# Optimization experiments

Hardware: AMD Instinct MI355X
Metric: run time of the kernel (lower is better)

The kernel has to match this reference:

```python
import jax, jax.numpy as jnp
import numpy as np

N = 50000          # nodes
E = 800000         # edges (avg in-degree 16)
IN_FEATS = 256
H = 4              # num_heads
D = 32             # out_feats per head
NEG_SLOPE = 0.2


def setup_inputs() -> dict:
    key = jax.random.key(0)
    k1, k2, k3, k4, k5, k6 = jax.random.split(key, 6)
    feat = jax.random.normal(k1, (N, IN_FEATS), dtype=jnp.float32)
    src = jax.random.randint(k2, (E,), 0, N, dtype=jnp.int32)
    dst = jax.random.randint(k3, (E,), 0, N, dtype=jnp.int32)
    # parameters (xavier-ish scale)
    W = jax.random.normal(k4, (IN_FEATS, H * D), dtype=jnp.float32) * (2.0 / (IN_FEATS + H * D)) ** 0.5
    attn_l = jax.random.normal(k5, (H, D), dtype=jnp.float32) * 0.1
    attn_r = jax.random.normal(k6, (H, D), dtype=jnp.float32) * 0.1
    bias = jnp.zeros((H * D,), dtype=jnp.float32)
    return {"feat": feat, "src": src, "dst": dst, "W": W,
            "attn_l": attn_l, "attn_r": attn_r, "bias": bias}


def reference(feat, src, dst, W, attn_l, attn_r, bias):
    # dense projection: [N, H, D]
    ft = (feat @ W).reshape(N, H, D)
    # per-node attention logits: [N, H]
    el = jnp.einsum('nhd,hd->nh', ft, attn_l)
    er = jnp.einsum('nhd,hd->nh', ft, attn_r)
    # SDDMM u_add_v + leaky relu: per-edge scores [E, H]
    e = jax.nn.leaky_relu(el[src] + er[dst], negative_slope=NEG_SLOPE)
    # edge softmax over incoming edges of each dst node (segment softmax)
    m = jax.ops.segment_max(e, dst, num_segments=N)          # [N, H], -inf for empty
    e_exp = jnp.exp(e - m[dst])                               # [E, H]
    s = jax.ops.segment_sum(e_exp, dst, num_segments=N)       # [N, H]
    a = e_exp / s[dst]                                        # [E, H]
    # SpMM u_mul_e: weighted aggregation to dst nodes
    rst = jax.ops.segment_sum(ft[src] * a[:, :, None], dst, num_segments=N)  # [N, H, D]
    rst = rst + bias.reshape(1, H, D)
    return rst
```

## Files before the change

### kernel.cpp

```cpp
#include <hip/hip_runtime.h>
#include <hip/hip_bf16.h>
#include <math.h>

#define N_NODES 50000
#define N_EDGES 800000
#define IN_F 256
#define HD 128
#define NHEAD 4
#define NB_SCAN 196

typedef __attribute__((ext_vector_type(8))) short bf16x8;
typedef __attribute__((ext_vector_type(4))) float f32x4;

__device__ __forceinline__ float lrelu(float x){ return x > 0.f ? x : 0.2f * x; }

__device__ __forceinline__ unsigned short f32_to_bf16_rn(float x){
    union { float f; unsigned int u; } v; v.f = x;
    unsigned int r = v.u + 0x7FFFu + ((v.u >> 16) & 1u);
    return (unsigned short)(r >> 16);
}
__device__ __forceinline__ float bf16_to_f32(unsigned short h){
    union { unsigned int u; float f; } v; v.u = ((unsigned int)h) << 16;
    return v.f;
}
__device__ __forceinline__ float bflo(unsigned int u){
    union { unsigned int x; float f; } v; v.x = u << 16; return v.f;
}
__device__ __forceinline__ float bfhi(unsigned int u){
    union { unsigned int x; float f; } v; v.x = u & 0xFFFF0000u; return v.f;
}

__global__ void zero_ints(int* __restrict__ p, int n){
    int i = blockIdx.x * blockDim.x + threadIdx.x;
    if (i < n) p[i] = 0;
}

__global__ __launch_bounds__(256) void wsplit_kernel(const float* __restrict__ W,
                                                     unsigned short* __restrict__ Wt_hi,
                                                     unsigned short* __restrict__ Wt_lo){
    int gid = blockIdx.x * 256 + threadIdx.x;
    int n = gid >> 8;
    int k = gid & 255;
    float x = W[(size_t)k * HD + n];
    unsigned short h = f32_to_bf16_rn(x);
    float r = x - bf16_to_f32(h);
    unsigned short l = f32_to_bf16_rn(r);
    Wt_hi[gid] = h;
    Wt_lo[gid] = l;
}

__global__ __launch_bounds__(256) void gemm_kernel(const float* __restrict__ feat,
                                                   const unsigned short* __restrict__ Wt_hi,
                                                   const unsigned short* __restrict__ Wt_lo,
                                                   const float* __restrict__ attn_l,
                                                   const float* __restrict__ attn_r,
                                                   unsigned short* __restrict__ ftb,
                                                   float* __restrict__ el,
                                                   float* __restrict__ er){
    __shared__ unsigned short Ah[128][72];
    __shared__ unsigned short Al[128][72];
    __shared__ unsigned short Bh[128][72];
    __shared__ unsigned short Bl[128][72];

    const int tid  = threadIdx.x;
    const int lane = tid & 63;
    const int wave = tid >> 6;
    const int wrow = wave * 32;
    const int lrow = lane & 15;
    const int lkh  = (lane >> 4) * 8;
    const int row0 = blockIdx.x * 128;

    f32x4 acc[2][8];
#pragma unroll
    for (int i = 0; i < 2; i++)
#pragma unroll
        for (int j = 0; j < 8; j++) acc[i][j] = (f32x4){0.f, 0.f, 0.f, 0.f};

    const int srow = tid >> 1;
    const int skh  = (tid & 1) * 32;

    for (int kc = 0; kc < 4; ++kc){
        const int k0 = kc * 64;
        {
            int gr = row0 + srow;
            const float* fp = feat + (size_t)gr * IN_F + k0 + skh;
            unsigned short* ah = &Ah[srow][skh];
            unsigned short* al = &Al[srow][skh];
#pragma unroll
            for (int u = 0; u < 8; ++u){
                float4 v = make_float4(0.f,0.f,0.f,0.f);
                if (gr < N_NODES) v = *(const float4*)(fp + 4 * u);
                ushort4 h, l;
                h.x = f32_to_bf16_rn(v.x); l.x = f32_to_bf16_rn(v.x - bf16_to_f32(h.x));
                h.y = f32_to_bf16_rn(v.y); l.y = f32_to_bf16_rn(v.y - bf16_to_f32(h.y));
                h.z = f32_to_bf16_rn(v.z); l.z = f32_to_bf16_rn(v.z - bf16_to_f32(h.z));
                h.w = f32_to_bf16_rn(v.w); l.w = f32_to_bf16_rn(v.w - bf16_to_f32(h.w));
                *(ushort4*)(ah + 4 * u) = h;
                *(ushort4*)(al + 4 * u) = l;
            }
        }
        {
            const unsigned short* bh = Wt_hi + srow * 256 + k0 + skh;
            const unsigned short* bl = Wt_lo + srow * 256 + k0 + skh;
#pragma unroll
            for (int u = 0; u < 4; ++u){
                *(uint4*)(&Bh[srow][skh + 8 * u]) = *(const uint4*)(bh + 8 * u);
                *(uint4*)(&Bl[srow][skh + 8 * u]) = *(const uint4*)(bl + 8 * u);
            }
        }
        __syncthreads();
#pragma unroll
        for (int kk = 0; kk < 2; ++kk){
            const int kb = kk * 32 + lkh;
            bf16x8 ah0 = *(const bf16x8*)(&Ah[wrow + lrow][kb]);
            bf16x8 ah1 = *(const bf16x8*)(&Ah[wrow + 16 + lrow][kb]);
            bf16x8 al0 = *(const bf16x8*)(&Al[wrow + lrow][kb]);
            bf16x8 al1 = *(const bf16x8*)(&Al[wrow + 16 + lrow][kb]);
#pragma unroll
            for (int nf = 0; nf < 8; ++nf){
                bf16x8 bh = *(const bf16x8*)(&Bh[nf * 16 + lrow][kb]);
                bf16x8 bl = *(const bf16x8*)(&Bl[nf * 16 + lrow][kb]);
                acc[0][nf] = __builtin_amdgcn_mfma_f32_16x16x32_bf16(ah0, bh, acc[0][nf], 0, 0, 0);
                acc[1][nf] = __builtin_amdgcn_mfma_f32_16x16x32_bf16(ah1, bh, acc[1][nf], 0, 0, 0);
                acc[0][nf] = __builtin_amdgcn_mfma_f32_16x16x32_bf16(ah0, bl, acc[0][nf], 0, 0, 0);
                acc[1][nf] = __builtin_amdgcn_mfma_f32_16x16x32_bf16(ah1, bl, acc[1][nf], 0, 0, 0);
                acc[0][nf] = __builtin_amdgcn_mfma_f32_16x16x32_bf16(al0, bh, acc[0][nf], 0, 0, 0);
                acc[1][nf] = __builtin_amdgcn_mfma_f32_16x16x32_bf16(al1, bh, acc[1][nf], 0, 0, 0);
            }
        }
        __syncthreads();
    }
    float alv[8], arv[8];
#pragma unroll
    for (int nf = 0; nf < 8; ++nf){
        alv[nf] = attn_l[lrow + nf * 16];
        arv[nf] = attn_r[lrow + nf * 16];
    }
#pragma unroll
    for (int mf = 0; mf < 2; ++mf){
#pragma unroll
        for (int r = 0; r < 4; ++r){
            int gr = row0 + wrow + mf * 16 + (lane >> 4) * 4 + r;
            if (gr < N_NODES){
                unsigned short* op = ftb + (size_t)gr * HD + lrow;
#pragma unroll
                for (int nf = 0; nf < 8; ++nf) op[nf * 16] = f32_to_bf16_rn(acc[mf][nf][r]);
            }
            float pl0 = acc[mf][0][r] * alv[0] + acc[mf][1][r] * alv[1];
            float pl1 = acc[mf][2][r] * alv[2] + acc[mf][3][r] * alv[3];
            float pl2 = acc[mf][4][r] * alv[4] + acc[mf][5][r] * alv[5];
            float pl3 = acc[mf][6][r] * alv[6] + acc[mf][7][r] * alv[7];
            float pr0 = acc[mf][0][r] * arv[0] + acc[mf][1][r] * arv[1];
            float pr1 = acc[mf][2][r] * arv[2] + acc[mf][3][r] * arv[3];
            float pr2 = acc[mf][4][r] * arv[4] + acc[mf][5][r] * arv[5];
            float pr3 = acc[mf][6][r] * arv[6] + acc[mf][7][r] * arv[7];
#pragma unroll
            for (int m = 1; m <= 8; m <<= 1){
                pl0 += __shfl_xor(pl0, m, 64); pl1 += __shfl_xor(pl1, m, 64);
                pl2 += __shfl_xor(pl2, m, 64); pl3 += __shfl_xor(pl3, m, 64);
                pr0 += __shfl_xor(pr0, m, 64); pr1 += __shfl_xor(pr1, m, 64);
                pr2 += __shfl_xor(pr2, m, 64); pr3 += __shfl_xor(pr3, m, 64);
            }
            if ((lane & 15) == 0 && gr < N_NODES){
                *(float4*)(el + (size_t)gr * NHEAD) = make_float4(pl0, pl1, pl2, pl3);
                *(float4*)(er + (size_t)gr * NHEAD) = make_float4(pr0, pr1, pr2, pr3);
            }
        }
    }
}

__global__ void degree_kernel(const int* __restrict__ dst, int* __restrict__ deg){
    int e = blockIdx.x * blockDim.x + threadIdx.x;
    if (e < N_EDGES) atomicAdd(&deg[dst[e]], 1);
}

__global__ __launch_bounds__(256) void scan_part(const int* __restrict__ deg,
                                                 int* __restrict__ row_off,
                                                 int* __restrict__ blk_sums){
    __shared__ int lds[256];
    int tid = threadIdx.x;
    int i = blockIdx.x * 256 + tid;
    int v = (i < N_NODES) ? deg[i] : 0;
    int x = v;
    lds[tid] = x;
    __syncthreads();
    for (int off = 1; off < 256; off <<= 1){
        int t = (tid >= off) ? lds[tid - off] : 0;
        __syncthreads();
        x += t;
        lds[tid] = x;
        __syncthreads();
    }
    if (i < N_NODES) row_off[i] = x - v;
    if (tid == 255) blk_sums[blockIdx.x] = x;
}

__global__ __launch_bounds__(256) void scan_mid(int* __restrict__ blk_sums,
                                                int* __restrict__ blk_off){
    __shared__ int lds[256];
    int tid = threadIdx.x;
    int v = (tid < NB_SCAN) ? blk_sums[tid] : 0;
    int x = v;
    lds[tid] = x;
    __syncthreads();
    for (int off = 1; off < 256; off <<= 1){
        int t = (tid >= off) ? lds[tid - off] : 0;
        __syncthreads();
        x += t;
        lds[tid] = x;
        __syncthreads();
    }
    blk_off[tid] = x - v;
}

__global__ __launch_bounds__(256) void scan_add(int* __restrict__ row_off,
                                                const int* __restrict__ blk_off){
    int i = blockIdx.x * 256 + threadIdx.x;
    if (i < N_NODES) row_off[i] += blk_off[blockIdx.x];
    if (blockIdx.x == 0 && threadIdx.x == 0) row_off[N_NODES] = N_EDGES;
}

__global__ void scatter_kernel(const int* __restrict__ src, const int* __restrict__ dst,
                               const float* __restrict__ el, const float* __restrict__ er,
                               const int* __restrict__ row_off, int* __restrict__ cursor,
                               int* __restrict__ csr_src, float* __restrict__ w_srt){
    int e = blockIdx.x * blockDim.x + threadIdx.x;
    if (e >= N_EDGES) return;
    int d = dst[e], s = src[e];
    int pos = row_off[d] + atomicAdd(&cursor[d], 1);
    csr_src[pos] = s;
    float4 elv = *(const float4*)(el + (size_t)s * NHEAD);
    float4 erv = *(const float4*)(er + (size_t)d * NHEAD);
    float4 w;
    w.x = __expf(lrelu(elv.x + erv.x));
    w.y = __expf(lrelu(elv.y + erv.y));
    w.z = __expf(lrelu(elv.z + erv.z));
    w.w = __expf(lrelu(elv.w + erv.w));
    *(float4*)(w_srt + (size_t)pos * NHEAD) = w;
}

__global__ __launch_bounds__(256) void aggregate_kernel(const unsigned short* __restrict__ ftb,
                                                        const int* __restrict__ csr_src,
                                                        const float* __restrict__ w_srt,
                                                        const int* __restrict__ row_off,
                                                        const float* __restrict__ bias,
                                                        float* __restrict__ out){
    int n    = blockIdx.x * 4 + (threadIdx.x >> 6);
    int lane = threadIdx.x & 63;
    int h    = lane >> 4;
    int beg  = row_off[n], end = row_off[n + 1];

    float a0 = 0.f, a1 = 0.f, ws = 0.f;
    int i = beg;
    for (; i + 4 <= end; i += 4){
        int s0 = csr_src[i + 0], s1 = csr_src[i + 1], s2 = csr_src[i + 2], s3 = csr_src[i + 3];
        float w0 = w_srt[(size_t)(i + 0) * NHEAD + h];
        float w1 = w_srt[(size_t)(i + 1) * NHEAD + h];
        float w2 = w_srt[(size_t)(i + 2) * NHEAD + h];
        float w3 = w_srt[(size_t)(i + 3) * NHEAD + h];
        unsigned int f0 = *(const unsigned int*)(ftb + (size_t)s0 * HD + 2 * lane);
        unsigned int f1 = *(const unsigned int*)(ftb + (size_t)s1 * HD + 2 * lane);
        unsigned int f2 = *(const unsigned int*)(ftb + (size_t)s2 * HD + 2 * lane);
        unsigned int f3 = *(const unsigned int*)(ftb + (size_t)s3 * HD + 2 * lane);
        a0 += w0 * bflo(f0) + w1 * bflo(f1) + w2 * bflo(f2) + w3 * bflo(f3);
        a1 += w0 * bfhi(f0) + w1 * bfhi(f1) + w2 * bfhi(f2) + w3 * bfhi(f3);
        ws += (w0 + w1) + (w2 + w3);
    }
    for (; i < end; ++i){
        int s = csr_src[i];
        float w = w_srt[(size_t)i * NHEAD + h];
        unsigned int f = *(const unsigned int*)(ftb + (size_t)s * HD + 2 * lane);
        a0 += w * bflo(f);
        a1 += w * bfhi(f);
        ws += w;
    }
    float inv = (end > beg) ? 1.f / ws : 0.f;
    float2 o;
    o.x = a0 * inv + bias[2 * lane + 0];
    o.y = a1 * inv + bias[2 * lane + 1];
    *(float2*)(out + (size_t)n * HD + 2 * lane) = o;
}

extern "C" void kernel_launch(void* const* d_in, const int* in_sizes, int n_in,
                              void* d_out, int out_size, void* d_ws, size_t ws_size,
                              hipStream_t stream){
    const float* feat   = (const float*)d_in[0];
    const int*   src    = (const int*)  d_in[1];
    const int*   dst    = (const int*)  d_in[2];
    const float* W      = (const float*)d_in[3];
    const float* attn_l = (const float*)d_in[4];
    const float* attn_r = (const float*)d_in[5];
    const float* bias   = (const float*)d_in[6];
    float* out = (float*)d_out;
    char*  ws  = (char*)d_ws;

    unsigned short* ftb = (unsigned short*)(ws + 0);
    float* el      = (float*)(ws + 12800000);
    float* er      = (float*)(ws + 13600000);
    int*   deg     = (int*)  (ws + 14400000);
    int*   cursor  = (int*)  (ws + 14600000);
    int*   row_off = (int*)  (ws + 14800000);
    int*   csr_src = (int*)  (ws + 15000064);
    float* w_srt   = (float*)(ws + 18200064);

    unsigned short* Wt_hi = (unsigned short*)csr_src;
    unsigned short* Wt_lo = Wt_hi + 32768;
    int* blk_sums = (int*)w_srt;
    int* blk_off  = blk_sums + 256;

    zero_ints<<<(2 * N_NODES + 255) / 256, 256, 0, stream>>>(deg, 2 * N_NODES);
    wsplit_kernel<<<128, 256, 0, stream>>>(W, Wt_hi, Wt_lo);
    gemm_kernel<<<(N_NODES + 127) / 128, 256, 0, stream>>>(feat, Wt_hi, Wt_lo,
                                                           attn_l, attn_r, ftb, el, er);
    degree_kernel<<<(N_EDGES + 255) / 256, 256, 0, stream>>>(dst, deg);
    scan_part<<<NB_SCAN, 256, 0, stream>>>(deg, row_off, blk_sums);
    scan_mid<<<1, 256, 0, stream>>>(blk_sums, blk_off);
    scan_add<<<NB_SCAN, 256, 0, stream>>>(row_off, blk_off);
    scatter_kernel<<<(N_EDGES + 255) / 256, 256, 0, stream>>>(src, dst, el, er,
                                                              row_off, cursor, csr_src, w_srt);
    aggregate_kernel<<<(N_NODES + 3) / 4, 256, 0, stream>>>(ftb, csr_src, w_srt,
                                                            row_off, bias, out);
}
```

Before: 253.6 us.

## Record edge rank in degree pass and compute edge weights inside aggregation

The degree kernel now stores each edge's atomic rank, so the scatter kernel places source indices without a second atomic cursor pass and no longer zeroes a cursor array. Edge attention weights are no longer computed and written per edge in the scatter. The aggregation kernel now computes them on the fly: each lane loads a source's el, applies leaky-relu and exp, and shares the weights across the wavefront by shuffles. This removes the w_srt write and read traffic and the second atomic pass, at the cost of storing a rank array and adding shuffles and a gather of el inside the aggregation loop.

```diff
diff --git a/kernel.cpp b/kernel.cpp
--- a/kernel.cpp
+++ b/kernel.cpp
@@ -169,9 +169,10 @@
     }
 }
 
-__global__ void degree_kernel(const int* __restrict__ dst, int* __restrict__ deg){
+__global__ void degree_kernel(const int* __restrict__ dst, int* __restrict__ deg,
+                              int* __restrict__ rank){
     int e = blockIdx.x * blockDim.x + threadIdx.x;
-    if (e < N_EDGES) atomicAdd(&deg[dst[e]], 1);
+    if (e < N_EDGES) rank[e] = atomicAdd(&deg[dst[e]], 1);
 }
 
 __global__ __launch_bounds__(256) void scan_part(const int* __restrict__ deg,
@@ -221,27 +222,17 @@
 }
 
 __global__ void scatter_kernel(const int* __restrict__ src, const int* __restrict__ dst,
-                               const float* __restrict__ el, const float* __restrict__ er,
-                               const int* __restrict__ row_off, int* __restrict__ cursor,
-                               int* __restrict__ csr_src, float* __restrict__ w_srt){
+                               const int* __restrict__ rank, const int* __restrict__ row_off,
+                               int* __restrict__ csr_src){
     int e = blockIdx.x * blockDim.x + threadIdx.x;
     if (e >= N_EDGES) return;
-    int d = dst[e], s = src[e];
-    int pos = row_off[d] + atomicAdd(&cursor[d], 1);
-    csr_src[pos] = s;
-    float4 elv = *(const float4*)(el + (size_t)s * NHEAD);
-    float4 erv = *(const float4*)(er + (size_t)d * NHEAD);
-    float4 w;
-    w.x = __expf(lrelu(elv.x + erv.x));
-    w.y = __expf(lrelu(elv.y + erv.y));
-    w.z = __expf(lrelu(elv.z + erv.z));
-    w.w = __expf(lrelu(elv.w + erv.w));
-    *(float4*)(w_srt + (size_t)pos * NHEAD) = w;
+    csr_src[row_off[dst[e]] + rank[e]] = src[e];
 }
 
 __global__ __launch_bounds__(256) void aggregate_kernel(const unsigned short* __restrict__ ftb,
                                                         const int* __restrict__ csr_src,
-                                                        const float* __restrict__ w_srt,
+                                                        const float* __restrict__ el,
+                                                        const float* __restrict__ er,
                                                         const int* __restrict__ row_off,
                                                         const float* __restrict__ bias,
                                                         float* __restrict__ out){
@@ -249,30 +240,34 @@
     int lane = threadIdx.x & 63;
     int h    = lane >> 4;
     int beg  = row_off[n], end = row_off[n + 1];
+    float4 ern = *(const float4*)(er + (size_t)n * NHEAD);
 
     float a0 = 0.f, a1 = 0.f, ws = 0.f;
-    int i = beg;
-    for (; i + 4 <= end; i += 4){
-        int s0 = csr_src[i + 0], s1 = csr_src[i + 1], s2 = csr_src[i + 2], s3 = csr_src[i + 3];
-        float w0 = w_srt[(size_t)(i + 0) * NHEAD + h];
-        float w1 = w_srt[(size_t)(i + 1) * NHEAD + h];
-        float w2 = w_srt[(size_t)(i + 2) * NHEAD + h];
-        float w3 = w_srt[(size_t)(i + 3) * NHEAD + h];
-        unsigned int f0 = *(const unsigned int*)(ftb + (size_t)s0 * HD + 2 * lane);
-        unsigned int f1 = *(const unsigned int*)(ftb + (size_t)s1 * HD + 2 * lane);
-        unsigned int f2 = *(const unsigned int*)(ftb + (size_t)s2 * HD + 2 * lane);
-        unsigned int f3 = *(const unsigned int*)(ftb + (size_t)s3 * HD + 2 * lane);
-        a0 += w0 * bflo(f0) + w1 * bflo(f1) + w2 * bflo(f2) + w3 * bflo(f3);
-        a1 += w0 * bfhi(f0) + w1 * bfhi(f1) + w2 * bfhi(f2) + w3 * bfhi(f3);
-        ws += (w0 + w1) + (w2 + w3);
-    }
-    for (; i < end; ++i){
-        int s = csr_src[i];
-        float w = w_srt[(size_t)i * NHEAD + h];
-        unsigned int f = *(const unsigned int*)(ftb + (size_t)s * HD + 2 * lane);
-        a0 += w * bflo(f);
-        a1 += w * bfhi(f);
-        ws += w;
+    for (int base = beg; base < end; base += 64){
+        int cnt = end - base; if (cnt > 64) cnt = 64;
+        int   s_l = 0;
+        float w0l = 0.f, w1l = 0.f, w2l = 0.f, w3l = 0.f;
+        if (lane < cnt){
+            s_l = csr_src[base + lane];
+            float4 elv = *(const float4*)(el + (size_t)s_l * NHEAD);
+            w0l = __expf(lrelu(elv.x + ern.x));
+            w1l = __expf(lrelu(elv.y + ern.y));
+            w2l = __expf(lrelu(elv.z + ern.z));
+            w3l = __expf(lrelu(elv.w + ern.w));
+        }
+#pragma unroll 4
+        for (int j = 0; j < cnt; ++j){
+            int s = __shfl(s_l, j, 64);
+            float w0 = __shfl(w0l, j, 64);
+            float w1 = __shfl(w1l, j, 64);
+            float w2 = __shfl(w2l, j, 64);
+            float w3 = __shfl(w3l, j, 64);
+            float w = (h == 0) ? w0 : (h == 1) ? w1 : (h == 2) ? w2 : w3;
+            unsigned int f = *(const unsigned int*)(ftb + (size_t)s * HD + 2 * lane);
+            a0 += w * bflo(f);
+            a1 += w * bfhi(f);
+            ws += w;
+        }
     }
     float inv = (end > beg) ? 1.f / ws : 0.f;
     float2 o;
@@ -298,26 +293,24 @@
     float* el      = (float*)(ws + 12800000);
     float* er      = (float*)(ws + 13600000);
     int*   deg     = (int*)  (ws + 14400000);
-    int*   cursor  = (int*)  (ws + 14600000);
-    int*   row_off = (int*)  (ws + 14800000);
-    int*   csr_src = (int*)  (ws + 15000064);
-    float* w_srt   = (float*)(ws + 18200064);
+    int*   rank    = (int*)  (ws + 14600000);
+    int*   row_off = (int*)  (ws + 17800000);
+    int*   csr_src = (int*)  (ws + 18000064);
 
     unsigned short* Wt_hi = (unsigned short*)csr_src;
     unsigned short* Wt_lo = Wt_hi + 32768;
-    int* blk_sums = (int*)w_srt;
+    int* blk_sums = (int*)(((char*)csr_src) + 131072);
     int* blk_off  = blk_sums + 256;
 
-    zero_ints<<<(2 * N_NODES + 255) / 256, 256, 0, stream>>>(deg, 2 * N_NODES);
+    zero_ints<<<(N_NODES + 255) / 256, 256, 0, stream>>>(deg, N_NODES);
     wsplit_kernel<<<128, 256, 0, stream>>>(W, Wt_hi, Wt_lo);
     gemm_kernel<<<(N_NODES + 127) / 128, 256, 0, stream>>>(feat, Wt_hi, Wt_lo,
                                                            attn_l, attn_r, ftb, el, er);
-    degree_kernel<<<(N_EDGES + 255) / 256, 256, 0, stream>>>(dst, deg);
+    degree_kernel<<<(N_EDGES + 255) / 256, 256, 0, stream>>>(dst, deg, rank);
     scan_part<<<NB_SCAN, 256, 0, stream>>>(deg, row_off, blk_sums);
     scan_mid<<<1, 256, 0, stream>>>(blk_sums, blk_off);
     scan_add<<<NB_SCAN, 256, 0, stream>>>(row_off, blk_off);
-    scatter_kernel<<<(N_EDGES + 255) / 256, 256, 0, stream>>>(src, dst, el, er,
-                                                              row_off, cursor, csr_src, w_srt);
-    aggregate_kernel<<<(N_NODES + 3) / 4, 256, 0, stream>>>(ftb, csr_src, w_srt,
+    scatter_kernel<<<(N_EDGES + 255) / 256, 256, 0, stream>>>(src, dst, rank, row_off, csr_src);
+    aggregate_kernel<<<(N_NODES + 3) / 4, 256, 0, stream>>>(ftb, csr_src, el, er,
                                                             row_off, bias, out);
 }
```

New measurement: 248.0 us. -2.2%, faster.
